# Kernel tuning notes

Hardware: AMD Instinct MI355X
Metric: run time of the kernel (lower is better)

The kernel has to match this reference:

```python
import jax, jax.numpy as jnp
import numpy as np

B, S, H, U = 32, 2048, 1024, 1024


def setup_inputs() -> dict:
    key = jax.random.key(0)
    ks = jax.random.split(key, 8)
    sH = 1.0 / np.sqrt(H)
    sU = 1.0 / np.sqrt(U)
    return {
        "encoder_output": jax.random.normal(ks[0], (B, S, H), dtype=jnp.float32),
        "last_layer_h_n": jax.random.normal(ks[1], (B, H), dtype=jnp.float32),
        # torch Linear stores weight [out,in]; we store transposed [in,out] for x @ W
        "W1_w": jax.random.uniform(ks[2], (H, U), jnp.float32, -sH, sH),
        "W1_b": jax.random.uniform(ks[3], (U,), jnp.float32, -sH, sH),
        "W2_w": jax.random.uniform(ks[4], (H, U), jnp.float32, -sH, sH),
        "W2_b": jax.random.uniform(ks[5], (U,), jnp.float32, -sH, sH),
        "V_w": jax.random.uniform(ks[6], (U, 1), jnp.float32, -sU, sU),
        "V_b": jax.random.uniform(ks[7], (1,), jnp.float32, -sU, sU),
    }


def reference(encoder_output, last_layer_h_n, W1_w, W1_b, W2_w, W2_b, V_w, V_b):
    # proj_enc: [B,S,U]; proj_h: [B,1,U] (unsqueeze(1) broadcast)
    proj_enc = jnp.einsum("bsh,hu->bsu", encoder_output, W1_w) + W1_b
    proj_h = (last_layer_h_n @ W2_w + W2_b)[:, None, :]
    # score: [B,S,1]
    score = jnp.tanh(proj_enc + proj_h) @ V_w + V_b
    # softmax over the sequence axis (dim 1)
    attention_weights = jax.nn.softmax(score, axis=1)
    # NOTE: in the original module context_vector is always None (dead branch),
    # so the faithful output is attention_weights alone.
    return attention_weights
```

## Files before the change

kernel.cpp:

```cpp
#include <hip/hip_runtime.h>
#include <hip/hip_bf16.h>


typedef __bf16 bf16x8 __attribute__((ext_vector_type(8)));
typedef float  f32x4  __attribute__((ext_vector_type(4)));

#define HDIM 1024
#define UDIM 1024
#define SDIM 2048
#define MROWS 65536
#define NT 16

__device__ inline unsigned short f2bf(float x) {
    return __builtin_bit_cast(unsigned short, (__bf16)x);
}

__device__ inline float fast_tanh(float x) {
    float z = __expf(-2.0f * __builtin_fabsf(x));
    float t = __fdividef(1.0f - z, 1.0f + z);
    return __builtin_copysignf(t, x);
}

#define GLDS16(gp, lp)                                                              \
    __builtin_amdgcn_global_load_lds(                                               \
        (const __attribute__((address_space(1))) unsigned int*)(gp),                \
        (__attribute__((address_space(3))) unsigned int*)(lp), 16, 0, 0)

__global__ __launch_bounds__(256) void cvt_kernel(const float* __restrict__ in,
                                                  unsigned short* __restrict__ out) {
    size_t i = ((size_t)blockIdx.x * 256 + threadIdx.x) * 8;
    const float4 f0 = *(const float4*)(in + i);
    const float4 f1 = *(const float4*)(in + i + 4);
    ushort4 h0, h1;
    h0.x = f2bf(f0.x); h0.y = f2bf(f0.y); h0.z = f2bf(f0.z); h0.w = f2bf(f0.w);
    h1.x = f2bf(f1.x); h1.y = f2bf(f1.y); h1.z = f2bf(f1.z); h1.w = f2bf(f1.w);
    *(ushort4*)(out + i) = h0;
    *(ushort4*)(out + i + 4) = h1;
}

__global__ void w1t_kernel(const float* __restrict__ W1, unsigned short* __restrict__ W1T) {
    __shared__ float tile[32][33];
    int bx = blockIdx.x;
    int by = blockIdx.y;
    int tx = threadIdx.x, ty = threadIdx.y;
#pragma unroll
    for (int r = 0; r < 4; ++r) {
        int h = by * 32 + ty + r * 8;
        int u = bx * 32 + tx;
        tile[ty + r * 8][tx] = W1[h * UDIM + u];
    }
    __syncthreads();
#pragma unroll
    for (int r = 0; r < 4; ++r) {
        int u = bx * 32 + ty + r * 8;
        int h = by * 32 + tx;
        W1T[u * HDIM + h] = f2bf(tile[tx][ty + r * 8]);
    }
}

__global__ void php_kernel(const float* __restrict__ hn, const float* __restrict__ W2,
                           float* __restrict__ php) {
    int u = (blockIdx.x & 3) * 256 + threadIdx.x;
    int b = blockIdx.y;
    int hc = blockIdx.z;
    int h0 = hc * 128;
    float acc = 0.f;
#pragma unroll 8
    for (int h = h0; h < h0 + 128; ++h)
        acc = fmaf(hn[b * HDIM + h], W2[h * UDIM + u], acc);
    php[(hc * 32 + b) * UDIM + u] = acc;
}

__global__ void ph_combine(const float* __restrict__ php, const float* __restrict__ W1b,
                           const float* __restrict__ W2b, float* __restrict__ ph) {
    int idx = blockIdx.x * 256 + threadIdx.x;
    int u = idx & (UDIM - 1);
    int b = idx >> 10;
    float acc = W1b[u] + W2b[u];
#pragma unroll
    for (int p = 0; p < 8; ++p) acc += php[(p * 32 + b) * UDIM + u];
    ph[idx] = acc;
}

__global__ __launch_bounds__(512, 2) void score_kernel2(
    const unsigned short* __restrict__ encb, const unsigned short* __restrict__ W1T,
    const float* __restrict__ ph, const float* __restrict__ Vw,
    float* __restrict__ part) {
    __shared__ __align__(16) unsigned short smem[65536];

    const int bx = blockIdx.x;
    const int x = bx & 7;
    const int k = bx >> 3;
    const int tile_n = k & 3;
    const int tile_m = (x << 5) | (k >> 2);
    const int row0 = tile_m * 256;
    const int col0 = tile_n * 256;

    const int t = threadIdx.x;
    const int lane = t & 63;
    const int wid = t >> 6;
    const int wm = wid >> 2;
    const int wn = wid & 3;

    const int e = lane & 7;
    const int c = lane >> 4;
    const int swz16 = (((c ^ (e & 3)) | ((e >> 2) << 2)) << 4);
    const int offk0 = ((lane & 15) << 7) + swz16;
    const int bhalf_off = (wn & 1) * 8192;

    const int rp0 = (wid << 3) + (lane >> 3);
    const int gsw = ((lane & 7) ^ (rp0 & 7)) << 3;
    const size_t gof0 = (size_t)rp0 * HDIM + gsw;
    const size_t gof1 = gof0 + (size_t)64 * HDIM;
    const unsigned lof0 = (unsigned)(wid << 10);
    const unsigned lof1 = lof0 + 8192u;

    const unsigned short* gA0 = encb + (size_t)row0 * HDIM;
    const unsigned short* gA1 = encb + (size_t)(row0 + 128) * HDIM;
    const unsigned short* gB0 = W1T + (size_t)col0 * HDIM;
    const unsigned short* gB1 = W1T + (size_t)(col0 + 128) * HDIM;

#define STAGE(gbase, kt, slotbyte)                                          \
    do {                                                                    \
        GLDS16((gbase) + (kt) + gof0, (char*)smem + (slotbyte) + lof0);     \
        GLDS16((gbase) + (kt) + gof1, (char*)smem + (slotbyte) + lof1);     \
    } while (0)

#define LOADA(half)                                                                          \
    _Pragma("unroll") for (int fi = 0; fi < 4; ++fi)                                         \
    _Pragma("unroll") for (int ks = 0; ks < 2; ++ks)                                         \
        aF[fi][ks] = *(const bf16x8*)((const char*)smem + slotA + ((half) + fi) * 2048 +     \
                                      (offk0 ^ (ks << 6)));

#define LOADB(dst, jhalf)                                                                    \
    _Pragma("unroll") for (int fj = 0; fj < 2; ++fj)                                         \
    _Pragma("unroll") for (int ks = 0; ks < 2; ++ks)                                         \
        dst[fj][ks] = *(const bf16x8*)((const char*)smem + slotB + bhalf_off +               \
                                       ((jhalf) + fj) * 2048 + (offk0 ^ (ks << 6)));

#define MFMA8(iBase, jBase, AF, BF)                                                          \
    _Pragma("unroll") for (int fi = 0; fi < 4; ++fi)                                         \
    _Pragma("unroll") for (int fj = 0; fj < 2; ++fj)                                         \
    _Pragma("unroll") for (int ks = 0; ks < 2; ++ks)                                         \
        acc[(iBase) + fi][(jBase) + fj] = __builtin_amdgcn_mfma_f32_16x16x32_bf16(           \
            AF[fi][ks], BF[fj][ks], acc[(iBase) + fi][(jBase) + fj], 0, 0, 0);

#define SBAR __builtin_amdgcn_s_barrier()

    f32x4 acc[8][4];
#pragma unroll
    for (int i = 0; i < 8; ++i)
#pragma unroll
        for (int j = 0; j < 4; ++j)
            acc[i][j] = (f32x4){0.f, 0.f, 0.f, 0.f};

    STAGE(gB0, 0, 0u);
    STAGE(gA0, 0, 16384u);
    STAGE(gA1, 0, 32768u);
    STAGE(gB1, 0, 49152u);
    STAGE(gB0, 64, 65536u);
    STAGE(gA0, 64, 81920u);
    asm volatile("s_waitcnt vmcnt(4)" ::: "memory");
    SBAR;

#pragma unroll 2
    for (int tau = 0; tau < NT; ++tau) {
        const unsigned sbase = (tau & 1) ? 65536u : 0u;
        const unsigned obase = 65536u - sbase;
        const unsigned slotA = sbase + (unsigned)(1 + wm) * 16384u;
        const unsigned slotB = sbase + ((wn & 2) ? 49152u : 0u);
        const int ktn1 = (tau + 1) * 64;
        const int ktn2 = (tau + 2) * 64;

        bf16x8 aF[4][2], bJ0[2][2], bJ1[2][2];

        LOADA(0);
        LOADB(bJ0, 0);
        if (tau + 1 < NT) STAGE(gA1, ktn1, obase + 32768u);
        SBAR;
        __builtin_amdgcn_s_setprio(1);
        MFMA8(0, 0, aF, bJ0);
        __builtin_amdgcn_s_setprio(0);
        SBAR;

        LOADB(bJ1, 2);
        if (tau + 1 < NT) STAGE(gB1, ktn1, obase + 49152u);
        SBAR;
        __builtin_amdgcn_s_setprio(1);
        MFMA8(0, 2, aF, bJ1);
        __builtin_amdgcn_s_setprio(0);
        SBAR;

        LOADA(4);
        if (tau + 2 < NT) STAGE(gB0, ktn2, sbase + 0u);
        SBAR;
        __builtin_amdgcn_s_setprio(1);
        MFMA8(4, 2, aF, bJ1);
        __builtin_amdgcn_s_setprio(0);
        SBAR;

        if (tau + 2 < NT) STAGE(gA0, ktn2, sbase + 16384u);
        SBAR;
        __builtin_amdgcn_s_setprio(1);
        MFMA8(4, 0, aF, bJ0);
        __builtin_amdgcn_s_setprio(0);
        if (tau < NT - 1) {
            if (tau == NT - 2) { asm volatile("s_waitcnt vmcnt(0)" ::: "memory"); }
            else               { asm volatile("s_waitcnt vmcnt(4)" ::: "memory"); }
            SBAR;
        }
    }

    __syncthreads();
    const int bidx = row0 >> 11;
    const int colg = lane & 15;
    const int rowq = (lane >> 4) << 2;
    float vw[4], phv[4];
#pragma unroll
    for (int j = 0; j < 4; ++j) {
        int u = col0 + wn * 64 + j * 16 + colg;
        vw[j] = Vw[u];
        phv[j] = ph[bidx * UDIM + u];
    }
    float* red = (float*)smem;
#pragma unroll
    for (int i = 0; i < 8; ++i) {
#pragma unroll
        for (int r = 0; r < 4; ++r) {
            float s = 0.f;
#pragma unroll
            for (int j = 0; j < 4; ++j) {
                float pe = acc[i][j][r] + phv[j];
                s += fast_tanh(pe) * vw[j];
            }
            s += __shfl_xor(s, 1);
            s += __shfl_xor(s, 2);
            s += __shfl_xor(s, 4);
            s += __shfl_xor(s, 8);
            if (colg == 0) red[wid * 128 + i * 16 + rowq + r] = s;
        }
    }
    __syncthreads();
    if (t < 256) {
        int wmr = t >> 7;
        int rl = t & 127;
        float s = red[(wmr * 4 + 0) * 128 + rl] + red[(wmr * 4 + 1) * 128 + rl] +
                  red[(wmr * 4 + 2) * 128 + rl] + red[(wmr * 4 + 3) * 128 + rl];
        part[(size_t)tile_n * MROWS + row0 + t] = s;
    }
#undef STAGE
#undef LOADA
#undef LOADB
#undef MFMA8
#undef SBAR
}

#define BM 128
#define BN 128
#define BK 32
#define LDK 40
__global__ __launch_bounds__(256) void score_kernel_f32(
    const float* __restrict__ enc, const unsigned short* __restrict__ W1T,
    const float* __restrict__ ph, const float* __restrict__ Vw,
    float* __restrict__ part) {
    __shared__ unsigned short As[BM * LDK];
    __shared__ unsigned short Bs[BN * LDK];

    const int bx = blockIdx.x;
    const int tile_n = bx & 7;
    const int tile_m = bx >> 3;
    const int t = threadIdx.x;
    const int lane = t & 63;
    const int wid = t >> 6;
    const int wm = wid >> 1, wn = wid & 1;

    const int row0 = tile_m * BM;
    const int col0 = tile_n * BN;

    f32x4 acc[4][4];
#pragma unroll
    for (int i = 0; i < 4; ++i)
#pragma unroll
        for (int j = 0; j < 4; ++j)
            acc[i][j] = (f32x4){0.f, 0.f, 0.f, 0.f};

    const int mrow = lane & 15;
    const int kq = (lane >> 4) * 8;

    for (int kt = 0; kt < HDIM; kt += BK) {
        __syncthreads();
#pragma unroll
        for (int i = 0; i < 4; ++i) {
            int cc = t + 256 * i;
            int r = cc >> 3;
            int kc = (cc & 7) * 4;
            const float4 f = *(const float4*)(enc + (size_t)(row0 + r) * HDIM + kt + kc);
            ushort4 h;
            h.x = f2bf(f.x); h.y = f2bf(f.y); h.z = f2bf(f.z); h.w = f2bf(f.w);
            *(ushort4*)(As + r * LDK + kc) = h;
        }
#pragma unroll
        for (int i = 0; i < 2; ++i) {
            int cc = t + 256 * i;
            int r = cc >> 2;
            int kc = (cc & 3) * 8;
            const uint4 v = *(const uint4*)(W1T + (size_t)(col0 + r) * HDIM + kt + kc);
            *(uint4*)(Bs + r * LDK + kc) = v;
        }
        __syncthreads();

        bf16x8 a[4], bb[4];
#pragma unroll
        for (int i = 0; i < 4; ++i)
            a[i] = *reinterpret_cast<const bf16x8*>(As + (wm * 64 + i * 16 + mrow) * LDK + kq);
#pragma unroll
        for (int j = 0; j < 4; ++j)
            bb[j] = *reinterpret_cast<const bf16x8*>(Bs + (wn * 64 + j * 16 + mrow) * LDK + kq);
#pragma unroll
        for (int i = 0; i < 4; ++i)
#pragma unroll
            for (int j = 0; j < 4; ++j)
                acc[i][j] = __builtin_amdgcn_mfma_f32_16x16x32_bf16(a[i], bb[j], acc[i][j], 0, 0, 0);
    }

    const int b = row0 >> 11;
    const int colg = lane & 15;
    const int rowq = (lane >> 4) * 4;
    float vw[4], phv[4];
#pragma unroll
    for (int j = 0; j < 4; ++j) {
        int u = col0 + wn * 64 + j * 16 + colg;
        vw[j] = Vw[u];
        phv[j] = ph[b * UDIM + u];
    }
#pragma unroll
    for (int i = 0; i < 4; ++i) {
#pragma unroll
        for (int r = 0; r < 4; ++r) {
            float s = 0.f;
#pragma unroll
            for (int j = 0; j < 4; ++j) {
                float pe = acc[i][j][r] + phv[j];
                s += fast_tanh(pe) * vw[j];
            }
            s += __shfl_xor(s, 1);
            s += __shfl_xor(s, 2);
            s += __shfl_xor(s, 4);
            s += __shfl_xor(s, 8);
            if (colg == 0) {
                int row = row0 + wm * 64 + i * 16 + rowq + r;
                part[(size_t)(tile_n * 2 + wn) * MROWS + row] = s;
            }
        }
    }
}

__global__ void softmax4_kernel(const float* __restrict__ part, float* __restrict__ out) {
    int b = blockIdx.x;
    int t = threadIdx.x;
    __shared__ float sred[4];
    float v[8];
    float lmax = -3.4e38f;
#pragma unroll
    for (int i = 0; i < 8; ++i) {
        int s = t + i * 256;
        float sum = 0.f;
#pragma unroll
        for (int p = 0; p < 4; ++p) sum += part[(size_t)p * MROWS + b * SDIM + s];
        v[i] = sum;
        lmax = fmaxf(lmax, sum);
    }
#pragma unroll
    for (int off = 1; off < 64; off <<= 1) lmax = fmaxf(lmax, __shfl_xor(lmax, off));
    if ((t & 63) == 0) sred[t >> 6] = lmax;
    __syncthreads();
    float bmax = fmaxf(fmaxf(sred[0], sred[1]), fmaxf(sred[2], sred[3]));
    __syncthreads();
    float lsum = 0.f;
#pragma unroll
    for (int i = 0; i < 8; ++i) {
        v[i] = expf(v[i] - bmax);
        lsum += v[i];
    }
#pragma unroll
    for (int off = 1; off < 64; off <<= 1) lsum += __shfl_xor(lsum, off);
    if ((t & 63) == 0) sred[t >> 6] = lsum;
    __syncthreads();
    float inv = 1.0f / (sred[0] + sred[1] + sred[2] + sred[3]);
#pragma unroll
    for (int i = 0; i < 8; ++i) out[b * SDIM + t + i * 256] = v[i] * inv;
}

__global__ void softmax16_kernel(const float* __restrict__ part, float* __restrict__ out) {
    int b = blockIdx.x;
    int t = threadIdx.x;
    __shared__ float sred[4];
    float v[8];
    float lmax = -3.4e38f;
#pragma unroll
    for (int i = 0; i < 8; ++i) {
        int s = t + i * 256;
        float sum = 0.f;
#pragma unroll
        for (int p = 0; p < 16; ++p) sum += part[(size_t)p * MROWS + b * SDIM + s];
        v[i] = sum;
        lmax = fmaxf(lmax, sum);
    }
#pragma unroll
    for (int off = 1; off < 64; off <<= 1) lmax = fmaxf(lmax, __shfl_xor(lmax, off));
    if ((t & 63) == 0) sred[t >> 6] = lmax;
    __syncthreads();
    float bmax = fmaxf(fmaxf(sred[0], sred[1]), fmaxf(sred[2], sred[3]));
    __syncthreads();
    float lsum = 0.f;
#pragma unroll
    for (int i = 0; i < 8; ++i) {
        v[i] = expf(v[i] - bmax);
        lsum += v[i];
    }
#pragma unroll
    for (int off = 1; off < 64; off <<= 1) lsum += __shfl_xor(lsum, off);
    if ((t & 63) == 0) sred[t >> 6] = lsum;
    __syncthreads();
    float inv = 1.0f / (sred[0] + sred[1] + sred[2] + sred[3]);
#pragma unroll
    for (int i = 0; i < 8; ++i) out[b * SDIM + t + i * 256] = v[i] * inv;
}

extern "C" void kernel_launch(void* const* d_in, const int* in_sizes, int n_in,
                              void* d_out, int out_size, void* d_ws, size_t ws_size,
                              hipStream_t stream) {
    const float* enc = (const float*)d_in[0];
    const float* hn  = (const float*)d_in[1];
    const float* W1  = (const float*)d_in[2];
    const float* W1b = (const float*)d_in[3];
    const float* W2  = (const float*)d_in[4];
    const float* W2b = (const float*)d_in[5];
    const float* Vw  = (const float*)d_in[6];
    float* out = (float*)d_out;

    char* ws = (char*)d_ws;
    const size_t ENCB_BYTES = (size_t)MROWS * HDIM * 2;
    const size_t NEED = ENCB_BYTES + (2u << 20) + (128u << 10) + (1u << 20) + (4u << 20);

    if (ws_size >= NEED) {
        unsigned short* encb = (unsigned short*)ws;
        unsigned short* W1T  = (unsigned short*)(ws + ENCB_BYTES);
        float* ph   = (float*)(ws + ENCB_BYTES + (2u << 20));
        float* php  = (float*)(ws + ENCB_BYTES + (2u << 20) + (128u << 10));
        float* part = (float*)(ws + ENCB_BYTES + (2u << 20) + (128u << 10) + (1u << 20));

        cvt_kernel<<<32768, 256, 0, stream>>>(enc, encb);
        w1t_kernel<<<dim3(32, 32), dim3(32, 8), 0, stream>>>(W1, W1T);
        php_kernel<<<dim3(4, 32, 8), 256, 0, stream>>>(hn, W2, php);
        ph_combine<<<128, 256, 0, stream>>>(php, W1b, W2b, ph);
        score_kernel2<<<dim3(1024), 512, 0, stream>>>(encb, W1T, ph, Vw, part);
        softmax4_kernel<<<32, 256, 0, stream>>>(part, out);
    } else {
        unsigned short* W1T = (unsigned short*)ws;
        float* ph   = (float*)(ws + (2u << 20));
        float* php  = (float*)(ws + (2u << 20) + (128u << 10));
        float* part = (float*)(ws + (2u << 20) + (128u << 10) + (1u << 20));

        w1t_kernel<<<dim3(32, 32), dim3(32, 8), 0, stream>>>(W1, W1T);
        php_kernel<<<dim3(4, 32, 8), 256, 0, stream>>>(hn, W2, php);
        ph_combine<<<128, 256, 0, stream>>>(php, W1b, W2b, ph);
        score_kernel_f32<<<dim3(4096), 256, 0, stream>>>(enc, W1T, ph, Vw, part);
        softmax16_kernel<<<32, 256, 0, stream>>>(part, out);
    }
}
```

Before: 550.7 us.

## Fuse fp32-to-bf16 conversion into score GEMM and make blocks persistent over M tiles

Removes the separate conversion kernel that wrote a bf16 copy of the encoder output. The score kernel now streams fp32 encoder rows directly into LDS via global_load_lds and converts to bf16 while loading MFMA fragments. Each of 256 blocks loops over four 256-row M tiles with a continuous 64-step K pipeline. This saves a full write and reread of the bf16 encoder tensor, but doubles the A-tile LDS footprint (about 132KB per block) and adds conversion work inside the inner loop.

```diff
diff --git a/kernel.cpp b/kernel.cpp
--- a/kernel.cpp
+++ b/kernel.cpp
@@ -9,7 +9,6 @@
 #define UDIM 1024
 #define SDIM 2048
 #define MROWS 65536
-#define NT 16
 
 __device__ inline unsigned short f2bf(float x) {
     return __builtin_bit_cast(unsigned short, (__bf16)x);
@@ -25,18 +24,6 @@
     __builtin_amdgcn_global_load_lds(                                               \
         (const __attribute__((address_space(1))) unsigned int*)(gp),                \
         (__attribute__((address_space(3))) unsigned int*)(lp), 16, 0, 0)
-
-__global__ __launch_bounds__(256) void cvt_kernel(const float* __restrict__ in,
-                                                  unsigned short* __restrict__ out) {
-    size_t i = ((size_t)blockIdx.x * 256 + threadIdx.x) * 8;
-    const float4 f0 = *(const float4*)(in + i);
-    const float4 f1 = *(const float4*)(in + i + 4);
-    ushort4 h0, h1;
-    h0.x = f2bf(f0.x); h0.y = f2bf(f0.y); h0.z = f2bf(f0.z); h0.w = f2bf(f0.w);
-    h1.x = f2bf(f1.x); h1.y = f2bf(f1.y); h1.z = f2bf(f1.z); h1.w = f2bf(f1.w);
-    *(ushort4*)(out + i) = h0;
-    *(ushort4*)(out + i + 4) = h1;
-}
 
 __global__ void w1t_kernel(const float* __restrict__ W1, unsigned short* __restrict__ W1T) {
     __shared__ float tile[32][33];
@@ -82,19 +69,17 @@
     ph[idx] = acc;
 }
 
-__global__ __launch_bounds__(512, 2) void score_kernel2(
-    const unsigned short* __restrict__ encb, const unsigned short* __restrict__ W1T,
+__global__ __launch_bounds__(512, 2) void score_kernel3(
+    const float* __restrict__ enc, const unsigned short* __restrict__ W1T,
     const float* __restrict__ ph, const float* __restrict__ Vw,
     float* __restrict__ part) {
-    __shared__ __align__(16) unsigned short smem[65536];
+    __shared__ __align__(16) char smem[135168];
 
     const int bx = blockIdx.x;
-    const int x = bx & 7;
-    const int k = bx >> 3;
-    const int tile_n = k & 3;
-    const int tile_m = (x << 5) | (k >> 2);
-    const int row0 = tile_m * 256;
-    const int col0 = tile_n * 256;
+    const int tile_n = bx & 3;
+    const int mgrp = bx >> 2;
+    const int arow0 = mgrp << 10;
+    const int col0 = tile_n << 8;
 
     const int t = threadIdx.x;
     const int lane = t & 63;
@@ -103,48 +88,76 @@
     const int wn = wid & 3;
 
     const int e = lane & 7;
-    const int c = lane >> 4;
-    const int swz16 = (((c ^ (e & 3)) | ((e >> 2) << 2)) << 4);
+    const int cc = lane >> 4;
+    const int swz16 = (((cc ^ (e & 3)) | ((e >> 2) << 2)) << 4);
     const int offk0 = ((lane & 15) << 7) + swz16;
     const int bhalf_off = (wn & 1) * 8192;
+    const unsigned slotB_q = ((wn & 2) ? 16384u : 0u);
+
+    const int mrow = lane & 15;
+    const int akc = (lane >> 4) << 1;
+    const int abase0 = mrow * 256 + ((akc ^ mrow) << 4);
+    const unsigned slotA = (unsigned)wm * 32768u;
 
     const int rp0 = (wid << 3) + (lane >> 3);
-    const int gsw = ((lane & 7) ^ (rp0 & 7)) << 3;
-    const size_t gof0 = (size_t)rp0 * HDIM + gsw;
-    const size_t gof1 = gof0 + (size_t)64 * HDIM;
-    const unsigned lof0 = (unsigned)(wid << 10);
-    const unsigned lof1 = lof0 + 8192u;
-
-    const unsigned short* gA0 = encb + (size_t)row0 * HDIM;
-    const unsigned short* gA1 = encb + (size_t)(row0 + 128) * HDIM;
-    const unsigned short* gB0 = W1T + (size_t)col0 * HDIM;
-    const unsigned short* gB1 = W1T + (size_t)(col0 + 128) * HDIM;
-
-#define STAGE(gbase, kt, slotbyte)                                          \
-    do {                                                                    \
-        GLDS16((gbase) + (kt) + gof0, (char*)smem + (slotbyte) + lof0);     \
-        GLDS16((gbase) + (kt) + gof1, (char*)smem + (slotbyte) + lof1);     \
+    const int gswB = ((lane & 7) ^ (rp0 & 7)) << 3;
+    const size_t gofB0 = (size_t)rp0 * HDIM + gswB;
+    const size_t gofB1 = gofB0 + (size_t)64 * HDIM;
+    const unsigned lofB0 = (unsigned)(wid << 10);
+    const unsigned lofB1 = lofB0 + 8192u;
+    const unsigned short* gB  = W1T + (size_t)col0 * HDIM;
+    const unsigned short* gB1g = gB + (size_t)128 * HDIM;
+
+#define BSLOT0(s) (((s) & 1) ? 98304u : 65536u)
+#define STAGE_B0(s)                                                          \
+    do {                                                                     \
+        const unsigned short* gp = gB + (((s) & 15) << 6);                   \
+        GLDS16(gp + gofB0, (char*)smem + BSLOT0(s) + lofB0);                 \
+        GLDS16(gp + gofB1, (char*)smem + BSLOT0(s) + lofB1);                 \
     } while (0)
-
-#define LOADA(half)                                                                          \
-    _Pragma("unroll") for (int fi = 0; fi < 4; ++fi)                                         \
-    _Pragma("unroll") for (int ks = 0; ks < 2; ++ks)                                         \
-        aF[fi][ks] = *(const bf16x8*)((const char*)smem + slotA + ((half) + fi) * 2048 +     \
-                                      (offk0 ^ (ks << 6)));
-
-#define LOADB(dst, jhalf)                                                                    \
-    _Pragma("unroll") for (int fj = 0; fj < 2; ++fj)                                         \
-    _Pragma("unroll") for (int ks = 0; ks < 2; ++ks)                                         \
-        dst[fj][ks] = *(const bf16x8*)((const char*)smem + slotB + bhalf_off +               \
-                                       ((jhalf) + fj) * 2048 + (offk0 ^ (ks << 6)));
-
-#define MFMA8(iBase, jBase, AF, BF)                                                          \
-    _Pragma("unroll") for (int fi = 0; fi < 4; ++fi)                                         \
-    _Pragma("unroll") for (int fj = 0; fj < 2; ++fj)                                         \
-    _Pragma("unroll") for (int ks = 0; ks < 2; ++ks)                                         \
-        acc[(iBase) + fi][(jBase) + fj] = __builtin_amdgcn_mfma_f32_16x16x32_bf16(           \
-            AF[fi][ks], BF[fj][ks], acc[(iBase) + fi][(jBase) + fj], 0, 0, 0);
-
+#define STAGE_B1(s)                                                          \
+    do {                                                                     \
+        const unsigned short* gp = gB1g + (((s) & 15) << 6);                 \
+        GLDS16(gp + gofB0, (char*)smem + BSLOT0(s) + 16384u + lofB0);        \
+        GLDS16(gp + gofB1, (char*)smem + BSLOT0(s) + 16384u + lofB1);        \
+    } while (0)
+#define STAGE_A(s)                                                           \
+    do {                                                                     \
+        const float* ga = enc +                                              \
+            (((size_t)(arow0 + (((s) >> 4) << 8))) << 10) + (((s) & 15) << 6); \
+        _Pragma("unroll") for (int i2 = 0; i2 < 4; ++i2) {                   \
+            const int ci = (wid << 8) + (i2 << 6) + lane;                    \
+            const int ri = ci >> 4, qi = ci & 15;                            \
+            const int gof = (ri << 10) + ((qi ^ (ri & 15)) << 2);            \
+            GLDS16(ga + gof, (char*)smem + (unsigned)(ci << 4));             \
+            GLDS16(ga + 131072 + gof, (char*)smem + 32768u + (unsigned)(ci << 4)); \
+        }                                                                    \
+    } while (0)
+#define LOADA(dst, fibase)                                                   \
+    _Pragma("unroll") for (int fi = 0; fi < 4; ++fi)                         \
+    _Pragma("unroll") for (int ks = 0; ks < 2; ++ks) {                       \
+        const unsigned o0 = slotA + (unsigned)((((fibase) + fi) << 12)) +    \
+                            (unsigned)(abase0 ^ (ks << 7));                  \
+        const f32x4 lo = *(const f32x4*)((const char*)smem + o0);            \
+        const f32x4 hi = *(const f32x4*)((const char*)smem + (o0 ^ 16u));    \
+        bf16x8 v;                                                            \
+        v[0] = (__bf16)lo[0]; v[1] = (__bf16)lo[1];                          \
+        v[2] = (__bf16)lo[2]; v[3] = (__bf16)lo[3];                          \
+        v[4] = (__bf16)hi[0]; v[5] = (__bf16)hi[1];                          \
+        v[6] = (__bf16)hi[2]; v[7] = (__bf16)hi[3];                          \
+        dst[fi][ks] = v;                                                     \
+    }
+#define LOADB(jhalf)                                                         \
+    _Pragma("unroll") for (int fj = 0; fj < 2; ++fj)                         \
+    _Pragma("unroll") for (int ks = 0; ks < 2; ++ks)                         \
+        bB[fj][ks] = *(const bf16x8*)((const char*)smem + slotB + bhalf_off + \
+                                      (((jhalf) + fj) << 11) + (offk0 ^ (ks << 6)));
+#define MFMA8(iBase, jBase, AF)                                              \
+    _Pragma("unroll") for (int fi = 0; fi < 4; ++fi)                         \
+    _Pragma("unroll") for (int fj = 0; fj < 2; ++fj)                         \
+    _Pragma("unroll") for (int ks = 0; ks < 2; ++ks)                         \
+        acc[(iBase) + fi][(jBase) + fj] = __builtin_amdgcn_mfma_f32_16x16x32_bf16( \
+            AF[fi][ks], bB[fj][ks], acc[(iBase) + fi][(jBase) + fj], 0, 0, 0);
 #define SBAR __builtin_amdgcn_s_barrier()
 
     f32x4 acc[8][4];
@@ -154,101 +167,111 @@
         for (int j = 0; j < 4; ++j)
             acc[i][j] = (f32x4){0.f, 0.f, 0.f, 0.f};
 
-    STAGE(gB0, 0, 0u);
-    STAGE(gA0, 0, 16384u);
-    STAGE(gA1, 0, 32768u);
-    STAGE(gB1, 0, 49152u);
-    STAGE(gB0, 64, 65536u);
-    STAGE(gA0, 64, 81920u);
-    asm volatile("s_waitcnt vmcnt(4)" ::: "memory");
+    STAGE_B0(0);
+    STAGE_A(0);
+    STAGE_B1(0);
+    STAGE_B0(1);
+    asm volatile("s_waitcnt vmcnt(0)" ::: "memory");
     SBAR;
 
+    for (int mt = 0; mt < 4; ++mt) {
 #pragma unroll 2
-    for (int tau = 0; tau < NT; ++tau) {
-        const unsigned sbase = (tau & 1) ? 65536u : 0u;
-        const unsigned obase = 65536u - sbase;
-        const unsigned slotA = sbase + (unsigned)(1 + wm) * 16384u;
-        const unsigned slotB = sbase + ((wn & 2) ? 49152u : 0u);
-        const int ktn1 = (tau + 1) * 64;
-        const int ktn2 = (tau + 2) * 64;
-
-        bf16x8 aF[4][2], bJ0[2][2], bJ1[2][2];
-
-        LOADA(0);
-        LOADB(bJ0, 0);
-        if (tau + 1 < NT) STAGE(gA1, ktn1, obase + 32768u);
-        SBAR;
-        __builtin_amdgcn_s_setprio(1);
-        MFMA8(0, 0, aF, bJ0);
-        __builtin_amdgcn_s_setprio(0);
-        SBAR;
-
-        LOADB(bJ1, 2);
-        if (tau + 1 < NT) STAGE(gB1, ktn1, obase + 49152u);
-        SBAR;
-        __builtin_amdgcn_s_setprio(1);
-        MFMA8(0, 2, aF, bJ1);
-        __builtin_amdgcn_s_setprio(0);
-        SBAR;
-
-        LOADA(4);
-        if (tau + 2 < NT) STAGE(gB0, ktn2, sbase + 0u);
-        SBAR;
-        __builtin_amdgcn_s_setprio(1);
-        MFMA8(4, 2, aF, bJ1);
-        __builtin_amdgcn_s_setprio(0);
-        SBAR;
-
-        if (tau + 2 < NT) STAGE(gA0, ktn2, sbase + 16384u);
-        SBAR;
-        __builtin_amdgcn_s_setprio(1);
-        MFMA8(4, 0, aF, bJ0);
-        __builtin_amdgcn_s_setprio(0);
-        if (tau < NT - 1) {
-            if (tau == NT - 2) { asm volatile("s_waitcnt vmcnt(0)" ::: "memory"); }
-            else               { asm volatile("s_waitcnt vmcnt(4)" ::: "memory"); }
-            SBAR;
-        }
-    }
-
-    __syncthreads();
-    const int bidx = row0 >> 11;
-    const int colg = lane & 15;
-    const int rowq = (lane >> 4) << 2;
-    float vw[4], phv[4];
-#pragma unroll
-    for (int j = 0; j < 4; ++j) {
-        int u = col0 + wn * 64 + j * 16 + colg;
-        vw[j] = Vw[u];
-        phv[j] = ph[bidx * UDIM + u];
-    }
-    float* red = (float*)smem;
-#pragma unroll
-    for (int i = 0; i < 8; ++i) {
-#pragma unroll
-        for (int r = 0; r < 4; ++r) {
-            float s = 0.f;
+        for (int tk = 0; tk < 16; ++tk) {
+            const int tau = (mt << 4) | tk;
+            const int s1 = tau + 1, s2 = tau + 2;
+            const unsigned bpar = (tk & 1) ? 98304u : 65536u;
+            const unsigned slotB = bpar + slotB_q;
+
+            bf16x8 aF0[4][2], aF1[4][2], bB[2][2];
+
+            LOADA(aF0, 0);
+            LOADB(0);
+            SBAR;
+            __builtin_amdgcn_s_setprio(1);
+            MFMA8(0, 0, aF0);
+            __builtin_amdgcn_s_setprio(0);
+            SBAR;
+
+            LOADA(aF1, 4);
+            if (s1 < 64) STAGE_B1(s1);
+            SBAR;
+            __builtin_amdgcn_s_setprio(1);
+            MFMA8(4, 0, aF1);
+            __builtin_amdgcn_s_setprio(0);
+            SBAR;
+
+            LOADB(2);
+            if (s1 < 64) STAGE_A(s1);
+            SBAR;
+            __builtin_amdgcn_s_setprio(1);
+            MFMA8(4, 2, aF1);
+            __builtin_amdgcn_s_setprio(0);
+            SBAR;
+
+            if (s2 < 64) STAGE_B0(s2);
+            SBAR;
+            __builtin_amdgcn_s_setprio(1);
+            MFMA8(0, 2, aF0);
+            __builtin_amdgcn_s_setprio(0);
+            if (tau < 62) {
+                asm volatile("s_waitcnt vmcnt(2)" ::: "memory");
+            } else if (tau == 62) {
+                asm volatile("s_waitcnt vmcnt(0)" ::: "memory");
+            }
+            SBAR;
+        }
+
+        __syncthreads();
+        {
+            float* red = (float*)(smem + 131072);
+            const int bidx = mgrp >> 1;
+            const int colg = lane & 15;
+            const int rowq = (lane >> 4) << 2;
+            float vw[4], phv[4];
 #pragma unroll
             for (int j = 0; j < 4; ++j) {
-                float pe = acc[i][j][r] + phv[j];
-                s += fast_tanh(pe) * vw[j];
-            }
-            s += __shfl_xor(s, 1);
-            s += __shfl_xor(s, 2);
-            s += __shfl_xor(s, 4);
-            s += __shfl_xor(s, 8);
-            if (colg == 0) red[wid * 128 + i * 16 + rowq + r] = s;
-        }
-    }
-    __syncthreads();
-    if (t < 256) {
-        int wmr = t >> 7;
-        int rl = t & 127;
-        float s = red[(wmr * 4 + 0) * 128 + rl] + red[(wmr * 4 + 1) * 128 + rl] +
-                  red[(wmr * 4 + 2) * 128 + rl] + red[(wmr * 4 + 3) * 128 + rl];
-        part[(size_t)tile_n * MROWS + row0 + t] = s;
-    }
-#undef STAGE
+                int u = col0 + wn * 64 + j * 16 + colg;
+                vw[j] = Vw[u];
+                phv[j] = ph[bidx * UDIM + u];
+            }
+#pragma unroll
+            for (int i = 0; i < 8; ++i) {
+#pragma unroll
+                for (int r = 0; r < 4; ++r) {
+                    float s = 0.f;
+#pragma unroll
+                    for (int j = 0; j < 4; ++j) {
+                        float pe = acc[i][j][r] + phv[j];
+                        s += fast_tanh(pe) * vw[j];
+                    }
+                    s += __shfl_xor(s, 1);
+                    s += __shfl_xor(s, 2);
+                    s += __shfl_xor(s, 4);
+                    s += __shfl_xor(s, 8);
+                    if (colg == 0) red[wid * 128 + i * 16 + rowq + r] = s;
+                }
+            }
+            __syncthreads();
+            if (t < 256) {
+                int wmr = t >> 7;
+                int rl = t & 127;
+                float s = red[(wmr * 4 + 0) * 128 + rl] + red[(wmr * 4 + 1) * 128 + rl] +
+                          red[(wmr * 4 + 2) * 128 + rl] + red[(wmr * 4 + 3) * 128 + rl];
+                part[(size_t)tile_n * MROWS + arow0 + (mt << 8) + t] = s;
+            }
+        }
+        if (mt < 3) {
+#pragma unroll
+            for (int i = 0; i < 8; ++i)
+#pragma unroll
+                for (int j = 0; j < 4; ++j)
+                    acc[i][j] = (f32x4){0.f, 0.f, 0.f, 0.f};
+        }
+    }
+#undef BSLOT0
+#undef STAGE_B0
+#undef STAGE_B1
+#undef STAGE_A
 #undef LOADA
 #undef LOADB
 #undef MFMA8
@@ -291,9 +314,9 @@
         __syncthreads();
 #pragma unroll
         for (int i = 0; i < 4; ++i) {
-            int cc = t + 256 * i;
-            int r = cc >> 3;
-            int kc = (cc & 7) * 4;
+            int ci = t + 256 * i;
+            int r = ci >> 3;
+            int kc = (ci & 7) * 4;
             const float4 f = *(const float4*)(enc + (size_t)(row0 + r) * HDIM + kt + kc);
             ushort4 h;
             h.x = f2bf(f.x); h.y = f2bf(f.y); h.z = f2bf(f.z); h.w = f2bf(f.w);
@@ -301,9 +324,9 @@
         }
 #pragma unroll
         for (int i = 0; i < 2; ++i) {
-            int cc = t + 256 * i;
-            int r = cc >> 2;
-            int kc = (cc & 3) * 8;
+            int ci = t + 256 * i;
+            int r = ci >> 2;
+            int kc = (ci & 3) * 8;
             const uint4 v = *(const uint4*)(W1T + (size_t)(col0 + r) * HDIM + kt + kc);
             *(uint4*)(Bs + r * LDK + kc) = v;
         }
@@ -440,21 +463,18 @@
     float* out = (float*)d_out;
 
     char* ws = (char*)d_ws;
-    const size_t ENCB_BYTES = (size_t)MROWS * HDIM * 2;
-    const size_t NEED = ENCB_BYTES + (2u << 20) + (128u << 10) + (1u << 20) + (4u << 20);
-
-    if (ws_size >= NEED) {
-        unsigned short* encb = (unsigned short*)ws;
-        unsigned short* W1T  = (unsigned short*)(ws + ENCB_BYTES);
-        float* ph   = (float*)(ws + ENCB_BYTES + (2u << 20));
-        float* php  = (float*)(ws + ENCB_BYTES + (2u << 20) + (128u << 10));
-        float* part = (float*)(ws + ENCB_BYTES + (2u << 20) + (128u << 10) + (1u << 20));
-
-        cvt_kernel<<<32768, 256, 0, stream>>>(enc, encb);
+    const size_t NEED = (2u << 20) + (128u << 10) + (1u << 20) + (1u << 20);
+
+    if (ws_size >= NEED + (1u << 20)) {
+        unsigned short* W1T = (unsigned short*)ws;
+        float* ph   = (float*)(ws + (2u << 20));
+        float* php  = (float*)(ws + (2u << 20) + (128u << 10));
+        float* part = (float*)(ws + (2u << 20) + (128u << 10) + (1u << 20));
+
         w1t_kernel<<<dim3(32, 32), dim3(32, 8), 0, stream>>>(W1, W1T);
         php_kernel<<<dim3(4, 32, 8), 256, 0, stream>>>(hn, W2, php);
         ph_combine<<<128, 256, 0, stream>>>(php, W1b, W2b, ph);
-        score_kernel2<<<dim3(1024), 512, 0, stream>>>(encb, W1T, ph, Vw, part);
+        score_kernel3<<<dim3(256), 512, 0, stream>>>(enc, W1T, ph, Vw, part);
         softmax4_kernel<<<32, 256, 0, stream>>>(part, out);
     } else {
         unsigned short* W1T = (unsigned short*)ws;
```

After: 1.104 ms. 100% more time.
